# Kernel tuning notes

Measured on AMD Instinct MI355X. Metric: run time of the kernel, lower is better.

The kernel has to match this reference:

```python
import jax, jax.numpy as jnp
import numpy as np
import math

N_EMBD = 1024
N_HEAD = 16
BLOCK_SIZE = 2048
B, T = 2, 2048


def setup_inputs() -> dict:
    key = jax.random.key(0)
    ks = jax.random.split(key, 12)
    s = 0.02
    C = N_EMBD
    return {
        "x": jax.random.normal(ks[0], (B, T, C), dtype=jnp.float32),
        # LayerNorm 1
        "ln1_w": jnp.ones((C,), jnp.float32),
        "ln1_b": jnp.zeros((C,), jnp.float32),
        # attention: weights stored [in, out]
        "attn_w": jax.random.normal(ks[1], (C, 3 * C), dtype=jnp.float32) * s,
        "attn_b": jnp.zeros((3 * C,), jnp.float32),
        "proj_w": jax.random.normal(ks[2], (C, C), dtype=jnp.float32) * s,
        "proj_b": jnp.zeros((C,), jnp.float32),
        # LayerNorm 2
        "ln2_w": jnp.ones((C,), jnp.float32),
        "ln2_b": jnp.zeros((C,), jnp.float32),
        # MLP
        "fc_w": jax.random.normal(ks[3], (C, 4 * C), dtype=jnp.float32) * s,
        "fc_b": jnp.zeros((4 * C,), jnp.float32),
        "mlp_proj_w": jax.random.normal(ks[4], (4 * C, C), dtype=jnp.float32) * s,
        "mlp_proj_b": jnp.zeros((C,), jnp.float32),
    }


def _layernorm(x, w, b, eps=1e-5):
    mu = jnp.mean(x, axis=-1, keepdims=True)
    var = jnp.mean(jnp.square(x - mu), axis=-1, keepdims=True)
    return (x - mu) * jax.lax.rsqrt(var + eps) * w + b


def _attention(x, attn_w, attn_b, proj_w, proj_b):
    Bn, Tn, C = x.shape
    hs = C // N_HEAD
    qkv = x @ attn_w + attn_b                      # [B,T,3C]
    q, k, v = jnp.split(qkv, 3, axis=-1)
    # [B,H,T,hs]
    q = q.reshape(Bn, Tn, N_HEAD, hs).transpose(0, 2, 1, 3)
    k = k.reshape(Bn, Tn, N_HEAD, hs).transpose(0, 2, 1, 3)
    v = v.reshape(Bn, Tn, N_HEAD, hs).transpose(0, 2, 1, 3)
    att = jnp.einsum('bhqd,bhkd->bhqk', q, k) / math.sqrt(hs)  # [B,H,T,T]
    mask = jnp.tril(jnp.ones((Tn, Tn), dtype=bool))
    att = jnp.where(mask, att, -jnp.inf)
    att = jax.nn.softmax(att, axis=-1)
    y = jnp.einsum('bhqk,bhkd->bhqd', att, v)      # [B,H,T,hs]
    y = y.transpose(0, 2, 1, 3).reshape(Bn, Tn, C)
    return y @ proj_w + proj_b


def reference(x, ln1_w, ln1_b, attn_w, attn_b, proj_w, proj_b,
              ln2_w, ln2_b, fc_w, fc_b, mlp_proj_w, mlp_proj_b):
    x = x + _attention(_layernorm(x, ln1_w, ln1_b), attn_w, attn_b, proj_w, proj_b)
    h = _layernorm(x, ln2_w, ln2_b)
    h = jax.nn.gelu(h @ fc_w + fc_b, approximate=False)  # torch nn.GELU default = exact erf
    return x + (h @ mlp_proj_w + mlp_proj_b)
```

## Files before the change

kernel.cpp:

```cpp
#include <hip/hip_runtime.h>
#include <math.h>

typedef short s8x __attribute__((ext_vector_type(8)));
typedef float f32x4 __attribute__((ext_vector_type(4)));
typedef int   i32x2 __attribute__((ext_vector_type(2)));

__device__ __forceinline__ float bf2f(short u) {
    return __uint_as_float(((unsigned int)(unsigned short)u) << 16);
}
__device__ __forceinline__ short f2bf(float f) {
    unsigned int x = __float_as_uint(f);
    unsigned int r = (x + 0x7FFFu + ((x >> 16) & 1u)) >> 16;
    return (short)(unsigned short)r;
}

__device__ __forceinline__ void gl2lds16(const short* g, const short* l) {
    __builtin_amdgcn_global_load_lds(
        (const __attribute__((address_space(1))) void*)(unsigned long long)g,
        (__attribute__((address_space(3))) void*)(unsigned int)(unsigned long long)l,
        16, 0, 0);
}

__device__ __forceinline__ void block_sync() {
    asm volatile("" ::: "memory");
    __builtin_amdgcn_s_barrier();
    asm volatile("" ::: "memory");
}
#define WAITV(n) asm volatile("s_waitcnt vmcnt(" #n ")" ::: "memory")

__device__ __forceinline__ void ln_row(const float* __restrict__ xin,
                                       const float* __restrict__ w,
                                       const float* __restrict__ bb,
                                       short* __restrict__ out, int row, int lane) {
    const float4* xr = (const float4*)(xin + (long)row * 1024);
    float4 v[4];
    float s1 = 0.f, s2 = 0.f;
#pragma unroll
    for (int i = 0; i < 4; ++i) {
        v[i] = xr[lane + i * 64];
        s1 += v[i].x + v[i].y + v[i].z + v[i].w;
        s2 += v[i].x*v[i].x + v[i].y*v[i].y + v[i].z*v[i].z + v[i].w*v[i].w;
    }
#pragma unroll
    for (int off = 32; off > 0; off >>= 1) {
        s1 += __shfl_xor(s1, off, 64);
        s2 += __shfl_xor(s2, off, 64);
    }
    const float mu = s1 * (1.0f / 1024.0f);
    float var = s2 * (1.0f / 1024.0f) - mu * mu;
    var = fmaxf(var, 0.0f);
    const float rs = rsqrtf(var + 1e-5f);
    short4* orow = (short4*)(out + (long)row * 1024);
#pragma unroll
    for (int i = 0; i < 4; ++i) {
        const int ci = (lane + i * 64) * 4;
        const float4 wv = *(const float4*)(w + ci);
        const float4 bv = *(const float4*)(bb + ci);
        short4 o;
        o.x = f2bf((v[i].x - mu) * rs * wv.x + bv.x);
        o.y = f2bf((v[i].y - mu) * rs * wv.y + bv.y);
        o.z = f2bf((v[i].z - mu) * rs * wv.z + bv.z);
        o.w = f2bf((v[i].w - mu) * rs * wv.w + bv.w);
        orow[lane + i * 64] = o;
    }
}

__global__ __launch_bounds__(256) void ln_k(const float* __restrict__ xin,
                                            const float* __restrict__ w,
                                            const float* __restrict__ bb,
                                            short* __restrict__ out) {
    ln_row(xin, w, bb, out, blockIdx.x * 4 + (threadIdx.x >> 6), threadIdx.x & 63);
}

__global__ __launch_bounds__(256) void pre_k(
        const float* __restrict__ w0, const float* __restrict__ w1,
        const float* __restrict__ w2, const float* __restrict__ w3,
        short* __restrict__ o0, short* __restrict__ o1,
        short* __restrict__ o2, short* __restrict__ o3,
        const float* __restrict__ x, const float* __restrict__ ln1w,
        const float* __restrict__ ln1b, short* __restrict__ xln) {
    int bid = blockIdx.x;
    if (bid >= 12288) {
        ln_row(x, ln1w, ln1b, xln, (bid - 12288) * 4 + (threadIdx.x >> 6), threadIdx.x & 63);
        return;
    }
    const float* in; short* out; int K, N, nx;
    if (bid < 3072)      { in = w0; out = o0; K = 1024; N = 3072; nx = 96; }
    else if (bid < 4096) { bid -= 3072; in = w1; out = o1; K = 1024; N = 1024; nx = 32; }
    else if (bid < 8192) { bid -= 4096; in = w2; out = o2; K = 1024; N = 4096; nx = 128; }
    else                 { bid -= 8192; in = w3; out = o3; K = 4096; N = 1024; nx = 32; }
    const int n0 = (bid % nx) * 32, k0 = (bid / nx) * 32;
    __shared__ float tile[32][33];
    const int tx = threadIdx.x & 31, ty = threadIdx.x >> 5;
#pragma unroll
    for (int i = 0; i < 4; ++i) {
        const int k = ty + i * 8;
        tile[k][tx] = in[(long)(k0 + k) * N + n0 + tx];
    }
    __syncthreads();
#pragma unroll
    for (int i = 0; i < 4; ++i) {
        const int n = ty + i * 8;
        out[(long)(n0 + n) * K + k0 + tx] = f2bf(tile[tx][n]);
    }
}

template <int EPI, typename OutT>
__device__ __forceinline__ void epi_store(OutT* out, const float* resid, long oidx, float v) {
    if constexpr (EPI == 0) {
        out[oidx] = f2bf(v);
    } else if constexpr (EPI == 1) {
        const float u = v * (0.79788456080f + 0.03567740814f * v * v);
        v = v / (1.0f + __expf(-2.0f * u));
        out[oidx] = f2bf(v);
    } else {
        v += resid[oidx];
        out[oidx] = v;
    }
}

template <int EPI, typename OutT>
__global__ __launch_bounds__(256) void gemm_k(const short* __restrict__ A,
                                              const short* __restrict__ Bt,
                                              const float* __restrict__ bias,
                                              const float* __restrict__ resid,
                                              OutT* __restrict__ out,
                                              int M, int N, int K) {
    __shared__ __align__(16) short sA[3][128 * 32];
    __shared__ __align__(16) short sB[3][128 * 32];
    const int tid = threadIdx.x;
    const int lane = tid & 63, wave = tid >> 6;
    const int wr = (wave >> 1) * 64, wc = (wave & 1) * 64;
    const int lrow = lane & 15, quad = lane >> 4;
    const int bm = blockIdx.y * 128, bn = blockIdx.x * 128;
    const short* Ap = A + (long)(bm + (tid >> 2)) * K + (tid & 3) * 8;
    const short* Bp = Bt + (long)(bn + (tid >> 2)) * K + (tid & 3) * 8;
    const long rowstep = (long)64 * K;

    auto stage = [&](int q, int k0) {
        gl2lds16(Ap + k0,           sA[q] + tid * 8);
        gl2lds16(Ap + rowstep + k0, sA[q] + 2048 + tid * 8);
        gl2lds16(Bp + k0,           sB[q] + tid * 8);
        gl2lds16(Bp + rowstep + k0, sB[q] + 2048 + tid * 8);
    };

    f32x4 acc[4][4] = {};
    const int S = K >> 5;
    stage(0, 0);
    stage(1, 32);
    int cur = 0, nx2 = 2;
    for (int s = 0; s < S; ++s) {
        if (s + 1 < S) { WAITV(4); } else { WAITV(0); }
        block_sync();
        if (s + 2 < S) stage(nx2, (s + 2) << 5);
        const short* pA = sA[cur];
        const short* pB = sB[cur];
        s8x af[4], bfr[4];
#pragma unroll
        for (int i = 0; i < 4; ++i) af[i]  = *(const s8x*)(pA + (wr + i*16 + lrow) * 32 + quad * 8);
#pragma unroll
        for (int j = 0; j < 4; ++j) bfr[j] = *(const s8x*)(pB + (wc + j*16 + lrow) * 32 + quad * 8);
#pragma unroll
        for (int i = 0; i < 4; ++i)
#pragma unroll
            for (int j = 0; j < 4; ++j)
                acc[i][j] = __builtin_amdgcn_mfma_f32_16x16x32_bf16(af[i], bfr[j], acc[i][j], 0, 0, 0);
        cur = (cur == 2) ? 0 : cur + 1;
        nx2 = (nx2 == 2) ? 0 : nx2 + 1;
    }
#pragma unroll
    for (int i = 0; i < 4; ++i) {
#pragma unroll
        for (int j = 0; j < 4; ++j) {
#pragma unroll
            for (int r = 0; r < 4; ++r) {
                const int row = bm + wr + i*16 + quad*4 + r;
                const int col = bn + wc + j*16 + lrow;
                epi_store<EPI>(out, resid, (long)row * N + col, acc[i][j][r] + bias[col]);
            }
        }
    }
}

template <int EPI, typename OutT>
__global__ __launch_bounds__(256) void gemm128x64_k(const short* __restrict__ A,
                                                    const short* __restrict__ Bt,
                                                    const float* __restrict__ bias,
                                                    const float* __restrict__ resid,
                                                    OutT* __restrict__ out,
                                                    int M, int N, int K) {
    __shared__ __align__(16) short sA[2][2][128 * 32];
    __shared__ __align__(16) short sB[2][2][64 * 32];
    const int tid = threadIdx.x;
    const int lane = tid & 63, wave = tid >> 6;
    const int wr = (wave >> 1) * 64, wc = (wave & 1) * 32;
    const int lrow = lane & 15, quad = lane >> 4;
    const int bm = blockIdx.y * 128, bn = blockIdx.x * 64;
    const short* Ap = A + (long)(bm + (tid >> 2)) * K + (tid & 3) * 8;
    const short* Bp = Bt + (long)(bn + (tid >> 2)) * K + (tid & 3) * 8;
    const long rowstep = (long)64 * K;

    auto stage = [&](int p, int k0) {
#pragma unroll
        for (int hp = 0; hp < 2; ++hp) {
            gl2lds16(Ap + k0 + hp * 32,           sA[p][hp] + tid * 8);
            gl2lds16(Ap + rowstep + k0 + hp * 32, sA[p][hp] + 2048 + tid * 8);
            gl2lds16(Bp + k0 + hp * 32,           sB[p][hp] + tid * 8);
        }
    };

    f32x4 acc[4][2] = {};
    stage(0, 0);
    const int S = K >> 6;
    for (int s = 0; s < S; ++s) {
        const int p = s & 1;
        __syncthreads();
        if (s + 1 < S) stage(p ^ 1, (s + 1) << 6);
#pragma unroll
        for (int hp = 0; hp < 2; ++hp) {
            s8x af[4], bfr[2];
#pragma unroll
            for (int i = 0; i < 4; ++i) af[i]  = *(const s8x*)(sA[p][hp] + (wr + i*16 + lrow) * 32 + quad * 8);
#pragma unroll
            for (int j = 0; j < 2; ++j) bfr[j] = *(const s8x*)(sB[p][hp] + (wc + j*16 + lrow) * 32 + quad * 8);
#pragma unroll
            for (int i = 0; i < 4; ++i)
#pragma unroll
                for (int j = 0; j < 2; ++j)
                    acc[i][j] = __builtin_amdgcn_mfma_f32_16x16x32_bf16(af[i], bfr[j], acc[i][j], 0, 0, 0);
        }
    }
#pragma unroll
    for (int i = 0; i < 4; ++i) {
#pragma unroll
        for (int j = 0; j < 2; ++j) {
#pragma unroll
            for (int r = 0; r < 4; ++r) {
                const int row = bm + wr + i*16 + quad*4 + r;
                const int col = bn + wc + j*16 + lrow;
                epi_store<EPI>(out, resid, (long)row * N + col, acc[i][j][r] + bias[col]);
            }
        }
    }
}

#define ATT_CS (0.125f * 1.4426950408889634f)
#define ATT_C0 (14.426950408889634f)

#define TR16(dst, off) \
    asm volatile("ds_read_b64_tr_b16 %0, %1 offset:" off : "=v"(dst) : "v"(tva))

__global__ __launch_bounds__(256) void attn_k(const short* __restrict__ qkv,
                                              short* __restrict__ y) {
    const int bx = blockIdx.x;
    const int b = blockIdx.y >> 4, h = blockIdx.y & 15;
    const int qtA = bx, qtB = 31 - bx;
    const int tid = threadIdx.x, lane = tid & 63, wave = tid >> 6;
    const int lrow = lane & 15, quad = lane >> 4;
    const long base = (long)b * 2048 * 3072;

    __shared__ __align__(16) short sK[3][64 * 64];
    __shared__ __align__(16) short sV[3][4096];

    s8x qfA0, qfA1, qfB0, qfB1;
    {
        const short* qpA = qkv + base + (long)(qtA * 64 + wave * 16 + lrow) * 3072 + h * 64 + quad * 8;
        qfA0 = *(const s8x*)qpA; qfA1 = *(const s8x*)(qpA + 32);
        const short* qpB = qkv + base + (long)(qtB * 64 + wave * 16 + lrow) * 3072 + h * 64 + quad * 8;
        qfB0 = *(const s8x*)qpB; qfB1 = *(const s8x*)(qpB + 32);
    }
    f32x4 oA[4], oB[4];
    float lA = 0.f, lB = 0.f;
#pragma unroll
    for (int d = 0; d < 4; ++d) { oA[d] = f32x4{0.f,0.f,0.f,0.f}; oB[d] = f32x4{0.f,0.f,0.f,0.f}; }

    const int srow = tid >> 3, sg = tid & 7;
    const int sw0 = ((srow & 7) ^ (srow >> 3)) & 7;
    const int sw1 = (((srow + 32) & 7) ^ ((srow + 32) >> 3)) & 7;
    const short* kbase = qkv + base + 1024 + h * 64;
    auto issueK = [&](int q, int k0) {
        gl2lds16(kbase + (long)(k0 + srow) * 3072      + (sg ^ sw0) * 8, sK[q] + tid * 8);
        gl2lds16(kbase + (long)(k0 + srow + 32) * 3072 + (sg ^ sw1) * 8, sK[q] + 2048 + tid * 8);
    };

    const int vslot   = (tid >> 3) & 7;
    const int vkbl    = 2 * (vslot & 3) + (vslot >> 2);
    const int vklocal = vkbl * 4 + ((tid >> 1) & 3);
    const short* vsrc = qkv + base + 2048 + h * 64
                      + (long)vklocal * 3072 + wave * 16 + 8 * (tid & 1);
    auto issueV = [&](int q, int k0) {
        gl2lds16(vsrc + (long)k0 * 3072,        sV[q] + tid * 8);
        gl2lds16(vsrc + (long)(k0 + 32) * 3072, sV[q] + 2048 + tid * 8);
    };
    const unsigned trb = (unsigned)(unsigned long long)(&sV[0][0]) + (unsigned)lane * 8u;

    auto tile_step = [&](const s8x& qf0, const s8x& qf1, const s8x* kf0, const s8x* kf1,
                         const s8x (*vfr)[4], f32x4* o, float& lsum, int qt, int kt, int k0) {
        f32x4 s[4];
#pragma unroll
        for (int ct = 0; ct < 4; ++ct) {
            f32x4 t = f32x4{0.f, 0.f, 0.f, 0.f};
            t = __builtin_amdgcn_mfma_f32_16x16x32_bf16(kf0[ct], qf0, t, 0, 0, 0);
            t = __builtin_amdgcn_mfma_f32_16x16x32_bf16(kf1[ct], qf1, t, 0, 0, 0);
            s[ct] = t;
        }
        const int qrow = qt * 64 + wave * 16 + lrow;
        float pv[4][4];
        if (kt == qt) {
#pragma unroll
            for (int ct = 0; ct < 4; ++ct)
#pragma unroll
                for (int r = 0; r < 4; ++r) {
                    const int key = k0 + ct * 16 + quad * 4 + r;
                    const float pp = exp2f(fmaf(s[ct][r], ATT_CS, -ATT_C0));
                    const float pt = __uint_as_float(__float_as_uint(pp) & 0xFFFF0000u);
                    pv[ct][r] = (key > qrow) ? 0.f : pt;
                }
        } else {
#pragma unroll
            for (int ct = 0; ct < 4; ++ct)
#pragma unroll
                for (int r = 0; r < 4; ++r) {
                    const float pp = exp2f(fmaf(s[ct][r], ATT_CS, -ATT_C0));
                    pv[ct][r] = __uint_as_float(__float_as_uint(pp) & 0xFFFF0000u);
                }
        }
#pragma unroll
        for (int ct = 0; ct < 4; ++ct)
            lsum += (pv[ct][0] + pv[ct][1]) + (pv[ct][2] + pv[ct][3]);

        unsigned int w2[4][2];
#pragma unroll
        for (int ct = 0; ct < 4; ++ct)
#pragma unroll
            for (int p2 = 0; p2 < 2; ++p2)
                w2[ct][p2] = __builtin_amdgcn_perm(__float_as_uint(pv[ct][2 * p2 + 1]),
                                                   __float_as_uint(pv[ct][2 * p2]), 0x07060302u);
        s8x pa[2];
#pragma unroll
        for (int ks = 0; ks < 2; ++ks) {
            auto rAC = __builtin_amdgcn_permlane32_swap((int)w2[2 * ks][0], (int)w2[2 * ks + 1][0], false, false);
            auto rBD = __builtin_amdgcn_permlane32_swap((int)w2[2 * ks][1], (int)w2[2 * ks + 1][1], false, false);
            auto mAC = __builtin_amdgcn_permlane16_swap(rAC[0], rAC[1], false, false);
            auto mBD = __builtin_amdgcn_permlane16_swap(rBD[0], rBD[1], false, false);
            int4 f;
            f.x = mAC[0]; f.y = mBD[0]; f.z = mAC[1]; f.w = mBD[1];
            pa[ks] = *(const s8x*)&f;
        }
#pragma unroll
        for (int ks = 0; ks < 2; ++ks)
#pragma unroll
            for (int dt = 0; dt < 4; ++dt)
                o[dt] = __builtin_amdgcn_mfma_f32_16x16x32_bf16(pa[ks], vfr[ks][dt], o[dt], 0, 0, 0);
    };

    issueK(0, 0);   issueV(0, 0);
    issueK(1, 64);  issueV(1, 64);
    int cur = 0, nx2 = 2;
    for (int kt = 0; kt <= qtB; ++kt) {
        const int k0 = kt * 64;
        if (kt < qtB) { WAITV(4); } else { WAITV(0); }
        block_sync();
        if (kt + 2 <= qtB) { issueK(nx2, k0 + 128); issueV(nx2, k0 + 128); }

        s8x kf0[4], kf1[4];
#pragma unroll
        for (int ct = 0; ct < 4; ++ct) {
            const int row = ct * 16 + lrow;
            const int swr = ((row & 7) ^ (row >> 3)) & 7;
            kf0[ct] = *(const s8x*)(sK[cur] + row * 64 + ((quad ^ swr) * 8));
            kf1[ct] = *(const s8x*)(sK[cur] + row * 64 + (((4 + quad) ^ swr) * 8));
        }

        const unsigned tva = trb + (unsigned)(cur << 13);
        i32x2 tr[16];
        TR16(tr[0],  "0");    TR16(tr[1],  "512");
        TR16(tr[2],  "1024"); TR16(tr[3],  "1536");
        TR16(tr[4],  "2048"); TR16(tr[5],  "2560");
        TR16(tr[6],  "3072"); TR16(tr[7],  "3584");
        TR16(tr[8],  "4096"); TR16(tr[9],  "4608");
        TR16(tr[10], "5120"); TR16(tr[11], "5632");
        TR16(tr[12], "6144"); TR16(tr[13], "6656");
        TR16(tr[14], "7168"); TR16(tr[15], "7680");
        asm volatile("s_waitcnt lgkmcnt(0)" ::: "memory");
        __builtin_amdgcn_sched_barrier(0);
        s8x vfr[2][4];
#pragma unroll
        for (int ks = 0; ks < 2; ++ks)
#pragma unroll
            for (int dt = 0; dt < 4; ++dt) {
                const int i2 = ks * 8 + dt * 2;
                int4 f;
                f.x = tr[i2][0]; f.y = tr[i2][1];
                f.z = tr[i2 + 1][0]; f.w = tr[i2 + 1][1];
                vfr[ks][dt] = *(const s8x*)&f;
            }

        if (kt <= qtA) tile_step(qfA0, qfA1, kf0, kf1, vfr, oA, lA, qtA, kt, k0);
        tile_step(qfB0, qfB1, kf0, kf1, vfr, oB, lB, qtB, kt, k0);

        cur = (cur == 2) ? 0 : cur + 1;
        nx2 = (nx2 == 2) ? 0 : nx2 + 1;
    }

    lA += __shfl_xor(lA, 16, 64); lA += __shfl_xor(lA, 32, 64);
    lB += __shfl_xor(lB, 16, 64); lB += __shfl_xor(lB, 32, 64);
    float rA[4], rB[4];
#pragma unroll
    for (int r = 0; r < 4; ++r) {
        rA[r] = 1.0f / __shfl(lA, quad * 4 + r, 64);
        rB[r] = 1.0f / __shfl(lB, quad * 4 + r, 64);
    }
#pragma unroll
    for (int dt = 0; dt < 4; ++dt) {
#pragma unroll
        for (int r = 0; r < 4; ++r) {
            const int qA = qtA * 64 + wave * 16 + quad * 4 + r;
            const int qB = qtB * 64 + wave * 16 + quad * 4 + r;
            y[((long)b * 2048 + qA) * 1024 + h * 64 + dt * 16 + lrow] = f2bf(oA[dt][r] * rA[r]);
            y[((long)b * 2048 + qB) * 1024 + h * 64 + dt * 16 + lrow] = f2bf(oB[dt][r] * rB[r]);
        }
    }
}

extern "C" void kernel_launch(void* const* d_in, const int* in_sizes, int n_in,
                              void* d_out, int out_size, void* d_ws, size_t ws_size,
                              hipStream_t stream) {
    const float* x      = (const float*)d_in[0];
    const float* ln1_w  = (const float*)d_in[1];
    const float* ln1_b  = (const float*)d_in[2];
    const float* attn_w = (const float*)d_in[3];
    const float* attn_b = (const float*)d_in[4];
    const float* proj_w = (const float*)d_in[5];
    const float* proj_b = (const float*)d_in[6];
    const float* ln2_w  = (const float*)d_in[7];
    const float* ln2_b  = (const float*)d_in[8];
    const float* fc_w   = (const float*)d_in[9];
    const float* fc_b   = (const float*)d_in[10];
    const float* mlp_w  = (const float*)d_in[11];
    const float* mlp_b  = (const float*)d_in[12];

    char* ws = (char*)d_ws;
    short* attn_wt = (short*)(ws + 0);
    short* proj_wt = (short*)(ws + 6291456L);
    short* fc_wt   = (short*)(ws + 8388608L);
    short* mlp_wt  = (short*)(ws + 16777216L);
    short* slotA   = (short*)(ws + 25165824L);
    short* slotB   = (short*)(ws + 33554432L);

    short* xln  = slotA;
    short* yb   = slotA;
    short* hb   = slotA;
    short* qkvb = slotB;
    short* hh   = slotB;
    float* x1   = (float*)d_out;
    float* outp = (float*)d_out;

    pre_k<<<13312, 256, 0, stream>>>(attn_w, proj_w, fc_w, mlp_w,
                                     attn_wt, proj_wt, fc_wt, mlp_wt,
                                     x, ln1_w, ln1_b, xln);

    gemm_k<0, short><<<dim3(24, 32), 256, 0, stream>>>(xln, attn_wt, attn_b, nullptr, qkvb, 4096, 3072, 1024);
    attn_k<<<dim3(16, 32), 256, 0, stream>>>(qkvb, yb);
    gemm128x64_k<2, float><<<dim3(16, 32), 256, 0, stream>>>(yb, proj_wt, proj_b, x, x1, 4096, 1024, 1024);
    ln_k<<<1024, 256, 0, stream>>>(x1, ln2_w, ln2_b, hb);
    gemm_k<1, short><<<dim3(32, 32), 256, 0, stream>>>(hb, fc_wt, fc_b, nullptr, hh, 4096, 4096, 1024);
    gemm128x64_k<3, float><<<dim3(16, 32), 256, 0, stream>>>(hh, mlp_wt, mlp_b, x1, outp, 4096, 1024, 4096);
}
```

Before: 337.0 us.

## Triple-buffer 128x64 GEMM with K=32 stages and swizzle block order

Restructures the 128x64 GEMM kernel's LDS pipeline from double-buffered 64-wide K steps to a three-stage ring of 32-wide K steps. Partial vmcnt waits let two loads stay in flight while the current tile is computed. It also remaps block IDs with an interleaving swizzle to improve L2 reuse of A/B tiles across concurrently running workgroups. The cost is twice as many barriers per K and less MFMA work between syncs. The swizzle assumes the workgroup count is divisible by 8.

```diff
diff --git a/kernel.cpp b/kernel.cpp
--- a/kernel.cpp
+++ b/kernel.cpp
@@ -189,46 +189,50 @@
                                                     const float* __restrict__ resid,
                                                     OutT* __restrict__ out,
                                                     int M, int N, int K) {
-    __shared__ __align__(16) short sA[2][2][128 * 32];
-    __shared__ __align__(16) short sB[2][2][64 * 32];
+    __shared__ __align__(16) short sA[3][128 * 32];
+    __shared__ __align__(16) short sB[3][64 * 32];
     const int tid = threadIdx.x;
     const int lane = tid & 63, wave = tid >> 6;
     const int wr = (wave >> 1) * 64, wc = (wave & 1) * 32;
     const int lrow = lane & 15, quad = lane >> 4;
-    const int bm = blockIdx.y * 128, bn = blockIdx.x * 64;
+    const int gx = gridDim.x;
+    const int nwg = gx * gridDim.y;
+    const int bid = blockIdx.y * gx + blockIdx.x;
+    const int swz = (bid & 7) * (nwg >> 3) + (bid >> 3);
+    const int bm = (swz / gx) * 128, bn = (swz % gx) * 64;
     const short* Ap = A + (long)(bm + (tid >> 2)) * K + (tid & 3) * 8;
     const short* Bp = Bt + (long)(bn + (tid >> 2)) * K + (tid & 3) * 8;
     const long rowstep = (long)64 * K;
 
-    auto stage = [&](int p, int k0) {
-#pragma unroll
-        for (int hp = 0; hp < 2; ++hp) {
-            gl2lds16(Ap + k0 + hp * 32,           sA[p][hp] + tid * 8);
-            gl2lds16(Ap + rowstep + k0 + hp * 32, sA[p][hp] + 2048 + tid * 8);
-            gl2lds16(Bp + k0 + hp * 32,           sB[p][hp] + tid * 8);
-        }
+    auto stage = [&](int q, int k0) {
+        gl2lds16(Ap + k0,           sA[q] + tid * 8);
+        gl2lds16(Ap + rowstep + k0, sA[q] + 2048 + tid * 8);
+        gl2lds16(Bp + k0,           sB[q] + tid * 8);
     };
 
     f32x4 acc[4][2] = {};
+    const int S = K >> 5;
     stage(0, 0);
-    const int S = K >> 6;
+    stage(1, 32);
+    int cur = 0, nx2 = 2;
     for (int s = 0; s < S; ++s) {
-        const int p = s & 1;
-        __syncthreads();
-        if (s + 1 < S) stage(p ^ 1, (s + 1) << 6);
-#pragma unroll
-        for (int hp = 0; hp < 2; ++hp) {
-            s8x af[4], bfr[2];
-#pragma unroll
-            for (int i = 0; i < 4; ++i) af[i]  = *(const s8x*)(sA[p][hp] + (wr + i*16 + lrow) * 32 + quad * 8);
-#pragma unroll
-            for (int j = 0; j < 2; ++j) bfr[j] = *(const s8x*)(sB[p][hp] + (wc + j*16 + lrow) * 32 + quad * 8);
-#pragma unroll
-            for (int i = 0; i < 4; ++i)
-#pragma unroll
-                for (int j = 0; j < 2; ++j)
-                    acc[i][j] = __builtin_amdgcn_mfma_f32_16x16x32_bf16(af[i], bfr[j], acc[i][j], 0, 0, 0);
-        }
+        if (s + 1 < S) { WAITV(3); } else { WAITV(0); }
+        block_sync();
+        if (s + 2 < S) stage(nx2, (s + 2) << 5);
+        const short* pA = sA[cur];
+        const short* pB = sB[cur];
+        s8x af[4], bfr[2];
+#pragma unroll
+        for (int i = 0; i < 4; ++i) af[i]  = *(const s8x*)(pA + (wr + i*16 + lrow) * 32 + quad * 8);
+#pragma unroll
+        for (int j = 0; j < 2; ++j) bfr[j] = *(const s8x*)(pB + (wc + j*16 + lrow) * 32 + quad * 8);
+#pragma unroll
+        for (int i = 0; i < 4; ++i)
+#pragma unroll
+            for (int j = 0; j < 2; ++j)
+                acc[i][j] = __builtin_amdgcn_mfma_f32_16x16x32_bf16(af[i], bfr[j], acc[i][j], 0, 0, 0);
+        cur = (cur == 2) ? 0 : cur + 1;
+        nx2 = (nx2 == 2) ? 0 : nx2 + 1;
     }
 #pragma unroll
     for (int i = 0; i < 4; ++i) {
```

After: 331.2 us. No clear change (-1.7%).
